# Optimization experiments

Measured on AMD Instinct MI355X. Metric: run time of the kernel, lower is better.

Reference implementation:

```python
import jax, jax.numpy as jnp
import numpy as np
import math

FILTER_SIZE = 11
FILTER_SIGMA = 1.5
C1 = 0.01 ** 2
C2 = 0.03 ** 2
PAD = FILTER_SIZE // 2


def _make_gauss_kernel(sigma, kernel_size, channel=3):
    mean = np.floor(0.5 * kernel_size)
    x = np.arange(kernel_size, dtype=np.float64)
    k1d = np.exp(-((x - mean) ** 2) / (2 * sigma ** 2)) * (1.0 / (2 * math.pi * sigma ** 2))
    k2d = np.outer(k1d, k1d).astype(np.float32)
    k2d = k2d / k2d.sum()
    # OIHW depthwise kernel: [channel, 1, k, k]
    return np.broadcast_to(k2d[None, None], (channel, 1, kernel_size, kernel_size)).copy()


def _depthwise_blur(x, kernel):
    # x: [B, 3, H, W], kernel: [3, 1, k, k]; groups=3, SAME padding (k//2)
    return jax.lax.conv_general_dilated(
        x, kernel,
        window_strides=(1, 1),
        padding=[(PAD, PAD), (PAD, PAD)],
        dimension_numbers=('NCHW', 'OIHW', 'NCHW'),
        feature_group_count=3,
    )


def setup_inputs() -> dict:
    key = jax.random.key(0)
    k1, k2 = jax.random.split(key)
    B, C, H, W = 32, 3, 512, 512
    image1 = jax.random.uniform(k1, (B, C, H, W), dtype=jnp.float32)
    image2 = jax.random.uniform(k2, (B, C, H, W), dtype=jnp.float32)
    gauss_kernel = jnp.asarray(_make_gauss_kernel(FILTER_SIGMA, FILTER_SIZE, channel=3))
    return {"image1": image1, "image2": image2, "gauss_kernel": gauss_kernel}


def reference(image1, image2, gauss_kernel):
    mu1 = _depthwise_blur(image1, gauss_kernel)
    mu2 = _depthwise_blur(image2, gauss_kernel)
    mu1_sq = mu1 * mu1
    mu2_sq = mu2 * mu2
    mu1_mu2 = mu1 * mu2
    sig1_sq = _depthwise_blur(image1 * image1, gauss_kernel) - mu1_sq
    sig2_sq = _depthwise_blur(image2 * image2, gauss_kernel) - mu2_sq
    sig1_sig2 = _depthwise_blur(image1 * image2, gauss_kernel) - mu1_mu2
    ssim_num = (2.0 * mu1_mu2 + C1) * (2.0 * sig1_sig2 + C2)
    ssim_den = (mu1_sq + mu2_sq + C1) * (sig1_sq + sig2_sq + C2)
    ssim_map = ssim_num / ssim_den
    dssim_map = (1.0 - ssim_map) * 0.5
    return dssim_map.mean()  # size_average=True
```

## Files before the change

### kernel.cpp

```cpp
#include <hip/hip_runtime.h>
#include <math.h>


namespace {
constexpr int IMG = 512;
constexpr int TW = 32;
constexpr int RB = 64;
constexpr int RING = RB + 10;
constexpr int SLOT = 32;
constexpr int XGN = TW / 8;
constexpr int SEGR = 128;
constexpr int NCHUNK = SEGR / RB;
constexpr int SEGN = IMG / SEGR;
constexpr int CTILES = IMG / TW;
constexpr int NIMG = 96;
constexpr float C1c = 1e-4f;
constexpr float C2c = 9e-4f;
constexpr float INV_N = 1.0f / 25165824.0f;
}

typedef float v2f __attribute__((ext_vector_type(2)));

__global__ void dssim_zero(float* ws) { ws[0] = 0.0f; }

__global__ void dssim_final(const float* __restrict__ ws, float* __restrict__ out) {
  out[0] = ws[0] * INV_N;
}

#define ACC_E(E, VA, VB) do {                                              \
    const int e_ = (E);                                                    \
    if (e_ >= 0 && e_ < 18) {                                              \
      float va_ = (VA), vb_ = (VB);                                        \
      float pab_ = va_ * vb_;                                              \
      float ps_  = __builtin_fmaf(vb_, vb_, va_ * va_);                    \
      v2f d01_; d01_.x = va_; d01_.y = vb_;                                \
      v2f d23_; d23_.x = ps_; d23_.y = pab_;                               \
      _Pragma("unroll")                                                    \
      for (int j_ = 0; j_ < 8; ++j_) {                                     \
        const int t_ = e_ - j_;                                            \
        if (t_ >= 0 && t_ < 11) {                                          \
          oab[j_] = __builtin_elementwise_fma(w2[t_], d01_, oab[j_]);      \
          osx[j_] = __builtin_elementwise_fma(w2[t_], d23_, osx[j_]);      \
        }                                                                  \
      }                                                                    \
    }                                                                      \
  } while (0)

__global__ __launch_bounds__(256, 4) void dssim_main(
    const float* __restrict__ im1, const float* __restrict__ im2,
    const float* __restrict__ gk, float* __restrict__ ws)
{
  __shared__ float sR[XGN * RING * SLOT];

  const int tid = threadIdx.x;
  const int bid = blockIdx.x;
  const int img = bid >> 6;
  const int rem = bid & 63;
  const int tsx = rem & 15;
  const int seg = rem >> 4;
  const int X0s = tsx * TW;
  const int Y0  = seg * SEGR;

  const float* __restrict__ p1 = im1 + (size_t)img * (IMG * IMG);
  const float* __restrict__ p2 = im2 + (size_t)img * (IMG * IMG);

  v2f w2[11];
  {
    float ic = 1.0f / sqrtf(gk[5 * 11 + 5]);
    #pragma unroll
    for (int t = 0; t < 11; ++t) {
      float w = gk[t * 11 + 5] * ic;
      w2[t].x = w; w2[t].y = w;
    }
  }

  const int c   = tid & 31;
  const int yg  = tid >> 5;
  const int xg3 = c >> 3;
  const int cl  = c & 7;

  float lsum = 0.f;

  for (int kc = 0; kc < NCHUNK; ++kc) {
    const int r0    = (kc == 0) ? -5 : RB * kc + 5;
    const int ntask = (kc == 0) ? XGN * RING : XGN * RB;
    for (int t = tid; t < ntask; t += 256) {
      const int xg = t & 3, dr = t >> 2;
      const int rl = r0 + dr;
      const int ry = Y0 + rl;
      const int rr = (rl + 5) % RING;
      const int cb = X0s + xg * 8 - 8;

      v2f oab[8], osx[8];
      #pragma unroll
      for (int j = 0; j < 8; ++j) { oab[j] = 0.f; osx[j] = 0.f; }

      if ((unsigned)ry < (unsigned)IMG) {
        const float* row1 = p1 + (size_t)ry * IMG;
        const float* row2 = p2 + (size_t)ry * IMG;
        if (cb >= 0 && cb + 24 <= IMG) {
          #pragma unroll
          for (int g = 0; g < 6; ++g) {
            float4 v1 = *(const float4*)(row1 + cb + 4 * g);
            float4 v2 = *(const float4*)(row2 + cb + 4 * g);
            ACC_E(4 * g - 3, v1.x, v2.x);
            ACC_E(4 * g - 2, v1.y, v2.y);
            ACC_E(4 * g - 1, v1.z, v2.z);
            ACC_E(4 * g + 0, v1.w, v2.w);
          }
        } else {
          #pragma unroll
          for (int i = 3; i <= 20; ++i) {
            int cc = cb + i;
            float va = 0.f, vb = 0.f;
            if ((unsigned)cc < (unsigned)IMG) { va = row1[cc]; vb = row2[cc]; }
            ACC_E(i - 3, va, vb);
          }
        }
      }

      const int base = (xg * RING + rr) * SLOT;
      const int rot  = 4 * (rr & 7) + 8 * xg;
      #pragma unroll
      for (int j = 0; j < 8; ++j) {
        const int a = base + ((4 * j + rot) & 31);
        *(v2f*)&sR[a]     = oab[j];
        *(v2f*)&sR[a + 2] = osx[j];
      }
    }
    __syncthreads();

    v2f mab[8], msx[8];
    #pragma unroll
    for (int j = 0; j < 8; ++j) { mab[j] = 0.f; msx[j] = 0.f; }

    const int y0l = RB * kc + yg * 8;
    int idx = y0l % RING;
    #pragma unroll
    for (int rr = 0; rr < 18; ++rr) {
      const int a = (xg3 * RING + idx) * SLOT +
                    ((4 * cl + 4 * (idx & 7) + 8 * xg3) & 31);
      float4 v4 = *(const float4*)&sR[a];
      v2f d01; d01.x = v4.x; d01.y = v4.y;
      v2f d23; d23.x = v4.z; d23.y = v4.w;
      #pragma unroll
      for (int j = 0; j < 8; ++j) {
        const int t = rr - j;
        if (t >= 0 && t < 11) {
          mab[j] = __builtin_elementwise_fma(w2[t], d01, mab[j]);
          msx[j] = __builtin_elementwise_fma(w2[t], d23, msx[j]);
        }
      }
      idx++; if (idx == RING) idx = 0;
    }

    #pragma unroll
    for (int j = 0; j < 8; ++j) {
      float m1 = mab[j].x, m2 = mab[j].y;
      float eS = msx[j].x, eX = msx[j].y;
      float m1s = m1 * m1, m2s = m2 * m2, m12 = m1 * m2;
      float sS  = eS - m1s - m2s;
      float s12 = eX - m12;
      float num = (2.f * m12 + C1c) * (2.f * s12 + C2c);
      float den = (m1s + m2s + C1c) * (sS + C2c);
      lsum += (1.f - num * __builtin_amdgcn_rcpf(den)) * 0.5f;
    }
    __syncthreads();
  }

  #pragma unroll
  for (int off = 32; off > 0; off >>= 1) lsum += __shfl_down(lsum, off);
  if ((tid & 63) == 0) sR[tid >> 6] = lsum;
  __syncthreads();
  if (tid == 0) atomicAdd(ws, sR[0] + sR[1] + sR[2] + sR[3]);
}

extern "C" void kernel_launch(void* const* d_in, const int* in_sizes, int n_in,
                              void* d_out, int out_size, void* d_ws, size_t ws_size,
                              hipStream_t stream) {
  const float* im1 = (const float*)d_in[0];
  const float* im2 = (const float*)d_in[1];
  const float* gk  = (const float*)d_in[2];
  float* out = (float*)d_out;
  float* ws  = (float*)d_ws;

  hipLaunchKernelGGL(dssim_zero, dim3(1), dim3(1), 0, stream, ws);
  hipLaunchKernelGGL(dssim_main, dim3(NIMG * CTILES * SEGN), dim3(256), 0, stream,
                     im1, im2, gk, ws);
  hipLaunchKernelGGL(dssim_final, dim3(1), dim3(1), 0, stream, ws, out);
}
```

Baseline: 267.1 us.

## Halve per-thread output tile in both blur passes, use smaller row chunks

The horizontal pass now gives each task 4 output columns instead of 8, using 8 column-slices per row. The vertical pass gives each thread 4 output rows instead of 8. Row chunks shrink from 64 to 32, giving a smaller ring buffer and more chunk iterations. This cuts register pressure and per-thread serial work and raises parallelism. In exchange, halo overhead grows: more redundant input loads and FMAs per output (14 taps for 4 outputs versus 18 for 8), plus more barriers.

Result: slower. 293.7 us (+10.0%).

```diff
diff --git a/kernel.cpp b/kernel.cpp
--- a/kernel.cpp
+++ b/kernel.cpp
@@ -5,12 +5,12 @@
 namespace {
 constexpr int IMG = 512;
 constexpr int TW = 32;
-constexpr int RB = 64;
-constexpr int RING = RB + 10;
+constexpr int HC = 32;
+constexpr int RING = HC + 10;
 constexpr int SLOT = 32;
 constexpr int XGN = TW / 8;
 constexpr int SEGR = 128;
-constexpr int NCHUNK = SEGR / RB;
+constexpr int NHC = SEGR / HC;
 constexpr int SEGN = IMG / SEGR;
 constexpr int CTILES = IMG / TW;
 constexpr int NIMG = 96;
@@ -29,14 +29,14 @@
 
 #define ACC_E(E, VA, VB) do {                                              \
     const int e_ = (E);                                                    \
-    if (e_ >= 0 && e_ < 18) {                                              \
+    if (e_ >= 0 && e_ < 14) {                                              \
       float va_ = (VA), vb_ = (VB);                                        \
       float pab_ = va_ * vb_;                                              \
       float ps_  = __builtin_fmaf(vb_, vb_, va_ * va_);                    \
       v2f d01_; d01_.x = va_; d01_.y = vb_;                                \
       v2f d23_; d23_.x = ps_; d23_.y = pab_;                               \
       _Pragma("unroll")                                                    \
-      for (int j_ = 0; j_ < 8; ++j_) {                                     \
+      for (int j_ = 0; j_ < 4; ++j_) {                                     \
         const int t_ = e_ - j_;                                            \
         if (t_ >= 0 && t_ < 11) {                                          \
           oab[j_] = __builtin_elementwise_fma(w2[t_], d01_, oab[j_]);      \
@@ -81,26 +81,28 @@
 
   float lsum = 0.f;
 
-  for (int kc = 0; kc < NCHUNK; ++kc) {
-    const int r0    = (kc == 0) ? -5 : RB * kc + 5;
-    const int ntask = (kc == 0) ? XGN * RING : XGN * RB;
+  for (int hc = 0; hc < NHC; ++hc) {
+    const int r0    = (hc == 0) ? -5 : HC * hc + 5;
+    const int ntask = (hc == 0) ? 8 * RING : 8 * HC;
     for (int t = tid; t < ntask; t += 256) {
-      const int xg = t & 3, dr = t >> 2;
+      const int cs = t & 7;
+      const int dr = t >> 3;
       const int rl = r0 + dr;
       const int ry = Y0 + rl;
-      const int rr = (rl + 5) % RING;
-      const int cb = X0s + xg * 8 - 8;
+      const int slot = (rl + 5) % RING;
+      const int xg = cs >> 1;
+      const int cb = X0s + 4 * cs - 8;
 
-      v2f oab[8], osx[8];
+      v2f oab[4], osx[4];
       #pragma unroll
-      for (int j = 0; j < 8; ++j) { oab[j] = 0.f; osx[j] = 0.f; }
+      for (int j = 0; j < 4; ++j) { oab[j] = 0.f; osx[j] = 0.f; }
 
       if ((unsigned)ry < (unsigned)IMG) {
         const float* row1 = p1 + (size_t)ry * IMG;
         const float* row2 = p2 + (size_t)ry * IMG;
-        if (cb >= 0 && cb + 24 <= IMG) {
+        if (cb >= 0 && cb + 16 <= IMG) {
           #pragma unroll
-          for (int g = 0; g < 6; ++g) {
+          for (int g = 0; g < 4; ++g) {
             float4 v1 = *(const float4*)(row1 + cb + 4 * g);
             float4 v2 = *(const float4*)(row2 + cb + 4 * g);
             ACC_E(4 * g - 3, v1.x, v2.x);
@@ -110,7 +112,7 @@
           }
         } else {
           #pragma unroll
-          for (int i = 3; i <= 20; ++i) {
+          for (int i = 3; i <= 16; ++i) {
             int cc = cb + i;
             float va = 0.f, vb = 0.f;
             if ((unsigned)cc < (unsigned)IMG) { va = row1[cc]; vb = row2[cc]; }
@@ -119,32 +121,33 @@
         }
       }
 
-      const int base = (xg * RING + rr) * SLOT;
-      const int rot  = 4 * (rr & 7) + 8 * xg;
+      const int base = (xg * RING + slot) * SLOT;
+      const int rot  = 4 * (slot & 7) + 8 * xg;
+      const int c0   = 4 * (cs & 1);
       #pragma unroll
-      for (int j = 0; j < 8; ++j) {
-        const int a = base + ((4 * j + rot) & 31);
+      for (int j = 0; j < 4; ++j) {
+        const int a = base + ((4 * (c0 + j) + rot) & 31);
         *(v2f*)&sR[a]     = oab[j];
         *(v2f*)&sR[a + 2] = osx[j];
       }
     }
     __syncthreads();
 
-    v2f mab[8], msx[8];
+    v2f mab[4], msx[4];
     #pragma unroll
-    for (int j = 0; j < 8; ++j) { mab[j] = 0.f; msx[j] = 0.f; }
+    for (int j = 0; j < 4; ++j) { mab[j] = 0.f; msx[j] = 0.f; }
 
-    const int y0l = RB * kc + yg * 8;
-    int idx = y0l % RING;
+    const int y0 = HC * hc + yg * 4;
+    int idx = y0 % RING;
     #pragma unroll
-    for (int rr = 0; rr < 18; ++rr) {
+    for (int rr = 0; rr < 14; ++rr) {
       const int a = (xg3 * RING + idx) * SLOT +
                     ((4 * cl + 4 * (idx & 7) + 8 * xg3) & 31);
       float4 v4 = *(const float4*)&sR[a];
       v2f d01; d01.x = v4.x; d01.y = v4.y;
       v2f d23; d23.x = v4.z; d23.y = v4.w;
       #pragma unroll
-      for (int j = 0; j < 8; ++j) {
+      for (int j = 0; j < 4; ++j) {
         const int t = rr - j;
         if (t >= 0 && t < 11) {
           mab[j] = __builtin_elementwise_fma(w2[t], d01, mab[j]);
@@ -155,7 +158,7 @@
     }
 
     #pragma unroll
-    for (int j = 0; j < 8; ++j) {
+    for (int j = 0; j < 4; ++j) {
       float m1 = mab[j].x, m2 = mab[j].y;
       float eS = msx[j].x, eX = msx[j].y;
       float m1s = m1 * m1, m2s = m2 * m2, m12 = m1 * m2;
```
